# Kernel optimization log

Hardware: AMD Instinct MI355X
Metric: run time of the kernel (lower is better)

Reference implementation:

```python
import jax, jax.numpy as jnp
import numpy as np

VOCAB_SIZE = 32128  # init kwarg vocab_size; one_hot=True so embedding_dim == vocab_size


def setup_inputs() -> dict:
    key = jax.random.key(0)
    x = jax.random.randint(key, (1024, 2048), 0, VOCAB_SIZE, dtype=jnp.int64 if jax.config.jax_enable_x64 else jnp.int32)
    return {"x": x}


def reference(x) -> jnp.ndarray:
    # Faithful math: one_hot(x, V).float().sum(axis=1) == per-row token-count
    # histogram. Implemented as a direct scatter-add into a (B, V) accumulator
    # instead of materializing the (B, S, V) one-hot tensor.
    B, S = x.shape
    rows = jnp.arange(B, dtype=x.dtype)[:, None]          # (B, 1) broadcast over seq
    out = jnp.zeros((B, VOCAB_SIZE), dtype=jnp.float32)
    out = out.at[rows, x].add(jnp.float32(1.0))           # (B, V) counts
    return out
```

## Files before the change

kernel.cpp:

```cpp
#include <hip/hip_runtime.h>


#define VOCAB 32128
#define WORDS (VOCAB / 2)
#define SEQ 2048
#define BLOCK 512

__global__ __launch_bounds__(BLOCK, 4) void hist_rows_kernel(
    const int* __restrict__ x, float* __restrict__ out) {
    __shared__ unsigned int cnt[WORDS];

    const int row = blockIdx.x;
    const int tid = threadIdx.x;

    uint4* c4 = reinterpret_cast<uint4*>(cnt);
    #pragma unroll
    for (int i = tid; i < WORDS / 4; i += BLOCK) {
        c4[i] = make_uint4(0u, 0u, 0u, 0u);
    }
    __syncthreads();

    const int4* xrow = reinterpret_cast<const int4*>(x + (size_t)row * SEQ);
    for (int i = tid; i < SEQ / 4; i += BLOCK) {
        int4 t = xrow[i];
        atomicAdd(&cnt[t.x >> 1], 1u << ((t.x & 1) * 16));
        atomicAdd(&cnt[t.y >> 1], 1u << ((t.y & 1) * 16));
        atomicAdd(&cnt[t.z >> 1], 1u << ((t.z & 1) * 16));
        atomicAdd(&cnt[t.w >> 1], 1u << ((t.w & 1) * 16));
    }
    __syncthreads();

    float4* orow = reinterpret_cast<float4*>(out + (size_t)row * VOCAB);
    const uint2* c2 = reinterpret_cast<const uint2*>(cnt);
    for (int i = tid; i < WORDS / 2; i += BLOCK) {
        uint2 w = c2[i];
        float4 f;
        f.x = (float)(w.x & 0xFFFFu);
        f.y = (float)(w.x >> 16);
        f.z = (float)(w.y & 0xFFFFu);
        f.w = (float)(w.y >> 16);
        orow[i] = f;
    }
}

extern "C" void kernel_launch(void* const* d_in, const int* in_sizes, int n_in,
                              void* d_out, int out_size, void* d_ws, size_t ws_size,
                              hipStream_t stream) {
    const int* x = (const int*)d_in[0];
    float* out = (float*)d_out;
    const int B = in_sizes[0] / SEQ;
    hipLaunchKernelGGL(hist_rows_kernel, dim3(B), dim3(BLOCK), 0, stream, x, out);
}
```

Before: 133.8 us.

## Split each row histogram into four vocab slices per block with nontemporal stores

Each row is now handled by four blocks, each owning a quarter of the vocabulary in a smaller shared-memory histogram. Every block reads the whole row and atomically counts only the tokens in its slice. This cuts LDS use per block, allowing more resident blocks and more parallelism. Output is written with nontemporal stores to avoid cache pollution. The cost is four times the input reads and wasted filtering work per token.

```diff
diff --git a/kernel.cpp b/kernel.cpp
--- a/kernel.cpp
+++ b/kernel.cpp
@@ -2,44 +2,57 @@
 
 
 #define VOCAB 32128
-#define WORDS (VOCAB / 2)
 #define SEQ 2048
-#define BLOCK 512
+#define SLICES 4
+#define SLICE_V (VOCAB / SLICES)
+#define SWORDS (SLICE_V / 2)
+#define BLOCK 256
 
-__global__ __launch_bounds__(BLOCK, 4) void hist_rows_kernel(
+typedef float f32x4 __attribute__((ext_vector_type(4)));
+
+__global__ __launch_bounds__(BLOCK, 8) void hist_slice_kernel(
     const int* __restrict__ x, float* __restrict__ out) {
-    __shared__ unsigned int cnt[WORDS];
+    __shared__ unsigned int cnt[SWORDS];
 
-    const int row = blockIdx.x;
-    const int tid = threadIdx.x;
+    const int bid   = blockIdx.x;
+    const int row   = bid >> 2;
+    const int slice = bid & 3;
+    const int tid   = threadIdx.x;
+    const unsigned base = (unsigned)(slice * SLICE_V);
+
+    const int4* xrow = reinterpret_cast<const int4*>(x + (size_t)row * SEQ);
+    int4 t0 = xrow[tid];
+    int4 t1 = xrow[tid + BLOCK];
 
     uint4* c4 = reinterpret_cast<uint4*>(cnt);
-    #pragma unroll
-    for (int i = tid; i < WORDS / 4; i += BLOCK) {
+    for (int i = tid; i < SWORDS / 4; i += BLOCK) {
         c4[i] = make_uint4(0u, 0u, 0u, 0u);
     }
     __syncthreads();
 
-    const int4* xrow = reinterpret_cast<const int4*>(x + (size_t)row * SEQ);
-    for (int i = tid; i < SEQ / 4; i += BLOCK) {
-        int4 t = xrow[i];
-        atomicAdd(&cnt[t.x >> 1], 1u << ((t.x & 1) * 16));
-        atomicAdd(&cnt[t.y >> 1], 1u << ((t.y & 1) * 16));
-        atomicAdd(&cnt[t.z >> 1], 1u << ((t.z & 1) * 16));
-        atomicAdd(&cnt[t.w >> 1], 1u << ((t.w & 1) * 16));
+    {
+        unsigned b;
+        b = (unsigned)t0.x - base; if (b < SLICE_V) atomicAdd(&cnt[b >> 1], 1u << ((b & 1) * 16));
+        b = (unsigned)t0.y - base; if (b < SLICE_V) atomicAdd(&cnt[b >> 1], 1u << ((b & 1) * 16));
+        b = (unsigned)t0.z - base; if (b < SLICE_V) atomicAdd(&cnt[b >> 1], 1u << ((b & 1) * 16));
+        b = (unsigned)t0.w - base; if (b < SLICE_V) atomicAdd(&cnt[b >> 1], 1u << ((b & 1) * 16));
+        b = (unsigned)t1.x - base; if (b < SLICE_V) atomicAdd(&cnt[b >> 1], 1u << ((b & 1) * 16));
+        b = (unsigned)t1.y - base; if (b < SLICE_V) atomicAdd(&cnt[b >> 1], 1u << ((b & 1) * 16));
+        b = (unsigned)t1.z - base; if (b < SLICE_V) atomicAdd(&cnt[b >> 1], 1u << ((b & 1) * 16));
+        b = (unsigned)t1.w - base; if (b < SLICE_V) atomicAdd(&cnt[b >> 1], 1u << ((b & 1) * 16));
     }
     __syncthreads();
 
-    float4* orow = reinterpret_cast<float4*>(out + (size_t)row * VOCAB);
+    float* orow = out + (size_t)row * VOCAB + base;
     const uint2* c2 = reinterpret_cast<const uint2*>(cnt);
-    for (int i = tid; i < WORDS / 2; i += BLOCK) {
+    for (int i = tid; i < SWORDS / 2; i += BLOCK) {
         uint2 w = c2[i];
-        float4 f;
+        f32x4 f;
         f.x = (float)(w.x & 0xFFFFu);
         f.y = (float)(w.x >> 16);
         f.z = (float)(w.y & 0xFFFFu);
         f.w = (float)(w.y >> 16);
-        orow[i] = f;
+        __builtin_nontemporal_store(f, reinterpret_cast<f32x4*>(orow) + i);
     }
 }
 
@@ -49,5 +62,5 @@
     const int* x = (const int*)d_in[0];
     float* out = (float*)d_out;
     const int B = in_sizes[0] / SEQ;
-    hipLaunchKernelGGL(hist_rows_kernel, dim3(B), dim3(BLOCK), 0, stream, x, out);
+    hipLaunchKernelGGL(hist_slice_kernel, dim3(B * SLICES), dim3(BLOCK), 0, stream, x, out);
 }
```

Result: slower. 141.1 us (+5.5%).

## Replace shared-memory histogram with global zero-fill plus global float atomics

Applied to the files above, without the earlier changes.

Drops the per-row LDS histogram with packed 16-bit counters. The new version launches a grid-stride kernel that zero-fills the whole output, then a scatter kernel that issues float atomicAdd directly into global memory for each token. This removes the large LDS allocation, which limited occupancy, and the LDS zeroing and conversion passes. In exchange it adds 2M global atomics and a second kernel launch, and the zero-fill is a separate write pass over the 131 MB output.

```diff
diff --git a/kernel.cpp b/kernel.cpp
--- a/kernel.cpp
+++ b/kernel.cpp
@@ -2,45 +2,37 @@
 
 
 #define VOCAB 32128
-#define WORDS (VOCAB / 2)
 #define SEQ 2048
-#define BLOCK 512
+#define BLOCK 256
 
-__global__ __launch_bounds__(BLOCK, 4) void hist_rows_kernel(
-    const int* __restrict__ x, float* __restrict__ out) {
-    __shared__ unsigned int cnt[WORDS];
+typedef float f32x4 __attribute__((ext_vector_type(4)));
 
+__global__ __launch_bounds__(BLOCK) void zero_out_kernel(float* __restrict__ out,
+                                                         int n_vec4) {
+    f32x4* o4 = reinterpret_cast<f32x4*>(out);
+    const f32x4 z = {0.f, 0.f, 0.f, 0.f};
+    int stride = gridDim.x * BLOCK;
+    for (int i = blockIdx.x * BLOCK + threadIdx.x; i < n_vec4; i += stride) {
+        o4[i] = z;
+    }
+}
+
+__global__ __launch_bounds__(BLOCK) void scatter_kernel(const int* __restrict__ x,
+                                                        float* __restrict__ out) {
     const int row = blockIdx.x;
     const int tid = threadIdx.x;
-
-    uint4* c4 = reinterpret_cast<uint4*>(cnt);
-    #pragma unroll
-    for (int i = tid; i < WORDS / 4; i += BLOCK) {
-        c4[i] = make_uint4(0u, 0u, 0u, 0u);
-    }
-    __syncthreads();
-
     const int4* xrow = reinterpret_cast<const int4*>(x + (size_t)row * SEQ);
-    for (int i = tid; i < SEQ / 4; i += BLOCK) {
-        int4 t = xrow[i];
-        atomicAdd(&cnt[t.x >> 1], 1u << ((t.x & 1) * 16));
-        atomicAdd(&cnt[t.y >> 1], 1u << ((t.y & 1) * 16));
-        atomicAdd(&cnt[t.z >> 1], 1u << ((t.z & 1) * 16));
-        atomicAdd(&cnt[t.w >> 1], 1u << ((t.w & 1) * 16));
-    }
-    __syncthreads();
-
-    float4* orow = reinterpret_cast<float4*>(out + (size_t)row * VOCAB);
-    const uint2* c2 = reinterpret_cast<const uint2*>(cnt);
-    for (int i = tid; i < WORDS / 2; i += BLOCK) {
-        uint2 w = c2[i];
-        float4 f;
-        f.x = (float)(w.x & 0xFFFFu);
-        f.y = (float)(w.x >> 16);
-        f.z = (float)(w.y & 0xFFFFu);
-        f.w = (float)(w.y >> 16);
-        orow[i] = f;
-    }
+    int4 t0 = xrow[tid];
+    int4 t1 = xrow[tid + BLOCK];
+    float* orow = out + (size_t)row * VOCAB;
+    atomicAdd(orow + t0.x, 1.0f);
+    atomicAdd(orow + t0.y, 1.0f);
+    atomicAdd(orow + t0.z, 1.0f);
+    atomicAdd(orow + t0.w, 1.0f);
+    atomicAdd(orow + t1.x, 1.0f);
+    atomicAdd(orow + t1.y, 1.0f);
+    atomicAdd(orow + t1.z, 1.0f);
+    atomicAdd(orow + t1.w, 1.0f);
 }
 
 extern "C" void kernel_launch(void* const* d_in, const int* in_sizes, int n_in,
@@ -49,5 +41,8 @@
     const int* x = (const int*)d_in[0];
     float* out = (float*)d_out;
     const int B = in_sizes[0] / SEQ;
-    hipLaunchKernelGGL(hist_rows_kernel, dim3(B), dim3(BLOCK), 0, stream, x, out);
+    const int n_vec4 = (B * VOCAB) / 4;
+
+    hipLaunchKernelGGL(zero_out_kernel, dim3(2048), dim3(BLOCK), 0, stream, out, n_vec4);
+    hipLaunchKernelGGL(scatter_kernel, dim3(B), dim3(BLOCK), 0, stream, x, out);
 }
```

Measured after the change: 232.5 us. 73.8% more time.
